# Kernel tuning notes

Hardware: AMD Instinct MI355X
Metric: run time of the kernel (lower is better)

Reference implementation:

```python
import jax, jax.numpy as jnp
import numpy as np

VOCAB = 16000
DIM = 1024
B, T = 4, 2048


def setup_inputs() -> dict:
    key = jax.random.key(0)
    k_ids, k_emb, k_w, k_lw, k_lb = jax.random.split(key, 5)
    input_ids = jax.random.randint(k_ids, (B, T), 0, VOCAB)
    embed = jax.random.normal(k_emb, (VOCAB, DIM), dtype=jnp.float32)
    # w_state = I + 0.05 * (default Linear init ~ U(-1/sqrt(dim), 1/sqrt(dim)))
    bound = 1.0 / np.sqrt(DIM)
    w_state = jnp.eye(DIM, dtype=jnp.float32) + 0.05 * jax.random.uniform(
        k_w, (DIM, DIM), minval=-bound, maxval=bound, dtype=jnp.float32)
    lm_w = jax.random.uniform(k_lw, (VOCAB, DIM), minval=-bound, maxval=bound, dtype=jnp.float32)
    lm_b = jax.random.uniform(k_lb, (VOCAB,), minval=-bound, maxval=bound, dtype=jnp.float32)
    return {"input_ids": input_ids, "embed": embed, "w_state": w_state,
            "lm_w": lm_w, "lm_b": lm_b}


def reference(input_ids, embed, w_state, lm_w, lm_b):
    # h: [B, T, D]
    h = embed[input_ids]
    state0 = jnp.zeros((h.shape[0], h.shape[2]), dtype=h.dtype)

    def step(state, h_t):
        # nn.Linear: state @ W^T ; then add input injection
        new_state = state @ w_state.T + h_t
        return new_state, new_state

    # scan over time: inputs [T, B, D]
    _, outs = jax.lax.scan(step, state0, jnp.swapaxes(h, 0, 1))
    hidden = jnp.swapaxes(outs, 0, 1)  # [B, T, D]
    logits = hidden @ lm_w.T + lm_b    # [B, T, V]
    return logits
```

## Files before the change

kernel.cpp:

```cpp
#include <hip/hip_runtime.h>
#include <hip/hip_bf16.h>
#include <stdint.h>

#define DD 1024
#define BB 4
#define TT 2048
#define VV 16000
#define LCH 8
#define NR 1024
#define PADR 512

typedef __bf16 bf16_t;
typedef float f32x4_t __attribute__((ext_vector_type(4)));
typedef bf16_t bf16x8_t __attribute__((ext_vector_type(8)));
typedef bf16_t bf16x4_t __attribute__((ext_vector_type(4)));

#define MODE_PLAIN 0
#define MODE_ROUND 1
#define MODE_LEVEL 2
#define MODE_CARRY 3

#define KIND_SQ 0
#define KIND_ROUND 1
#define KIND_LEVEL 2
#define KIND_CARRY 3

struct Job {
  const float* A; const float* B; float* C; const float* Cin;
  int kind; int dlt;
};
struct Jobs { Job j[8]; };

__global__ __launch_bounds__(256) void k_cvt(const float* __restrict__ src,
                                             bf16_t* __restrict__ dst, int n4) {
  int i = blockIdx.x * blockDim.x + threadIdx.x;
  int stride = gridDim.x * blockDim.x;
  for (; i < n4; i += stride) {
    float4 v = ((const float4*)src)[i];
    union { ushort4 u; bf16_t h[4]; } p;
    p.h[0] = (bf16_t)v.x; p.h[1] = (bf16_t)v.y;
    p.h[2] = (bf16_t)v.z; p.h[3] = (bf16_t)v.w;
    ((ushort4*)dst)[i] = p.u;
  }
}

__global__ __launch_bounds__(256) void k_gather(const float* __restrict__ embed,
                                                const int* __restrict__ ids,
                                                float* __restrict__ slab0) {
  int r = blockIdx.x;
  int b = r & 3, c = r >> 2;
  int id = ids[b * TT + c * LCH];
  const float4* s = (const float4*)(embed + (size_t)id * DD);
  float4* d = (float4*)(slab0 + (size_t)r * DD);
  for (int i = threadIdx.x; i < DD / 4; i += blockDim.x) d[i] = s[i];
}

template <int NS>
__device__ __forceinline__ void swrite(char* base, int byteoff, float4 v) {
  float r0 = v.x, r1 = v.y, r2 = v.z, r3 = v.w;
#pragma unroll
  for (int p = 0; p < NS; ++p) {
    bf16x4_t h;
    h[0] = (bf16_t)r0; h[1] = (bf16_t)r1; h[2] = (bf16_t)r2; h[3] = (bf16_t)r3;
    *(bf16x4_t*)(base + p * 5120 + byteoff) = h;
    if (p + 1 < NS) {
      r0 -= (float)h[0]; r1 -= (float)h[1]; r2 -= (float)h[2]; r3 -= (float)h[3];
    }
  }
}

template <int NS, bool NN, int MODE>
__device__ __forceinline__ void mbody(bf16_t* __restrict__ SB, const Job& jb,
                                      const float* __restrict__ embed,
                                      const int* __restrict__ ids,
                                      bf16_t* __restrict__ hidden) {
  const float* A = jb.A;
  const float* Bm = jb.B;
  const int tid = threadIdx.x, lane = tid & 63, wave = tid >> 6;
  const int i0 = blockIdx.y * 64, j0 = blockIdx.x * 64;
  const int wm = (wave >> 1) * 32, wn = (wave & 1) * 32;
  char* Ap = (char*)SB;
  char* Bp = Ap + NS * 5120;
  const int arow = tid >> 2;
  const int akb = (tid & 3) * 8;
  const int bj = tid & 63, bk4 = (tid >> 6) * 4;
  const int frow = lane & 15, fkb = (lane >> 4) * 16;
  f32x4_t acc[2][2] = {};

  const float* Aptr = A + (size_t)(i0 + arow) * DD + (tid & 3) * 4;
  const float* BptrNT = Bm + (size_t)(j0 + arow) * DD + (tid & 3) * 4;
  const float* BptrNN = Bm + (size_t)bk4 * DD + j0 + bj;

  float4 a0 = *(const float4*)(Aptr);
  float4 a1 = *(const float4*)(Aptr + 16);
  float4 b0, b1;
  float s0[4], s1[4];
  if (!NN) {
    b0 = *(const float4*)(BptrNT);
    b1 = *(const float4*)(BptrNT + 16);
  } else {
#pragma unroll
    for (int s = 0; s < 4; ++s) s0[s] = BptrNN[(size_t)s * DD];
#pragma unroll
    for (int s = 0; s < 4; ++s) s1[s] = BptrNN[(size_t)(16 + s) * DD];
  }

  for (int k0 = 0;;) {
    __syncthreads();
    swrite<NS>(Ap, arow * 80 + akb, a0);
    swrite<NS>(Ap, arow * 80 + akb + 32, a1);
    if (!NN) {
      swrite<NS>(Bp, arow * 80 + akb, b0);
      swrite<NS>(Bp, arow * 80 + akb + 32, b1);
    } else {
      float4 t0; t0.x = s0[0]; t0.y = s0[1]; t0.z = s0[2]; t0.w = s0[3];
      float4 t1; t1.x = s1[0]; t1.y = s1[1]; t1.z = s1[2]; t1.w = s1[3];
      swrite<NS>(Bp, bj * 80 + bk4 * 2, t0);
      swrite<NS>(Bp, bj * 80 + bk4 * 2 + 32, t1);
    }
    __syncthreads();
    int kn = k0 + 32;
    if (kn < DD) {
      a0 = *(const float4*)(Aptr + kn);
      a1 = *(const float4*)(Aptr + kn + 16);
      if (!NN) {
        b0 = *(const float4*)(BptrNT + kn);
        b1 = *(const float4*)(BptrNT + kn + 16);
      } else {
#pragma unroll
        for (int s = 0; s < 4; ++s) s0[s] = BptrNN[(size_t)(kn + s) * DD];
#pragma unroll
        for (int s = 0; s < 4; ++s) s1[s] = BptrNN[(size_t)(kn + 16 + s) * DD];
      }
    }
    bf16x8_t af[NS][2], bfx[NS][2];
#pragma unroll
    for (int p = 0; p < NS; ++p)
#pragma unroll
      for (int mf = 0; mf < 2; ++mf) {
        af[p][mf] = *(const bf16x8_t*)(Ap + p * 5120 + (wm + mf * 16 + frow) * 80 + fkb);
        bfx[p][mf] = *(const bf16x8_t*)(Bp + p * 5120 + (wn + mf * 16 + frow) * 80 + fkb);
      }
#pragma unroll
    for (int pa = 0; pa < NS; ++pa)
#pragma unroll
      for (int pb = 0; pb < NS; ++pb) {
        if (pa + pb < NS) {
#pragma unroll
          for (int mf = 0; mf < 2; ++mf)
#pragma unroll
            for (int nf = 0; nf < 2; ++nf)
              acc[mf][nf] = __builtin_amdgcn_mfma_f32_16x16x32_bf16(
                  af[pa][mf], bfx[pb][nf], acc[mf][nf], 0, 0, 0);
        }
      }
    k0 = kn;
    if (k0 >= DD) break;
  }

  const int ecol = lane & 15, er4 = (lane >> 4) * 4;
#pragma unroll
  for (int mf = 0; mf < 2; ++mf) {
#pragma unroll
    for (int nf = 0; nf < 2; ++nf) {
      const int rb = i0 + wm + mf * 16 + er4;
      const int cj = j0 + wn + nf * 16 + ecol;
#pragma unroll
      for (int rg = 0; rg < 4; ++rg) {
        const int ri = rb + rg;
        float v = acc[mf][nf][rg];
        if (MODE == MODE_PLAIN) {
          jb.C[(size_t)ri * DD + cj] = v;
        } else if (MODE == MODE_ROUND) {
          int b = ri & 3, c = ri >> 2, t = c * LCH + jb.dlt;
          v += embed[(size_t)ids[b * TT + t] * DD + cj];
          jb.C[(size_t)ri * DD + cj] = v;
        } else if (MODE == MODE_LEVEL) {
          v += jb.Cin[(size_t)ri * DD + cj];
          jb.C[(size_t)ri * DD + cj] = v;
        } else {
          int b = ri & 3, c = ri >> 2, t = c * LCH + jb.dlt;
          hidden[((size_t)b * TT + t) * DD + cj] =
              (bf16_t)(v + jb.Cin[(size_t)ri * DD + cj]);
        }
      }
    }
  }
}

__global__ __launch_bounds__(256, 2) void k_multi(Jobs jobs,
                                                  const float* __restrict__ embed,
                                                  const int* __restrict__ ids,
                                                  bf16_t* __restrict__ hidden) {
  __shared__ __align__(16) bf16_t SB[6 * 2560];
  const Job& jb = jobs.j[blockIdx.z];
  if (jb.kind == KIND_SQ)
    mbody<3, true, MODE_PLAIN>(SB, jb, embed, ids, hidden);
  else if (jb.kind == KIND_ROUND)
    mbody<2, false, MODE_ROUND>(SB, jb, embed, ids, hidden);
  else if (jb.kind == KIND_LEVEL)
    mbody<2, false, MODE_LEVEL>(SB, jb, embed, ids, hidden);
  else
    mbody<2, false, MODE_CARRY>(SB, jb, embed, ids, hidden);
}

__device__ __forceinline__ void gload16(const void* g, void* l) {
  __builtin_amdgcn_global_load_lds((const __attribute__((address_space(1))) void*)g,
                                   (__attribute__((address_space(3))) void*)l, 16, 0, 0);
}

__global__ __launch_bounds__(256) void k_lmhead(const bf16_t* __restrict__ Ah,
                                                const bf16_t* __restrict__ Bw,
                                                const float* __restrict__ bias,
                                                float* __restrict__ Cout) {
  __shared__ bf16_t Al[128 * 64];
  __shared__ bf16_t Bl[128 * 64];
  int orig = blockIdx.y * gridDim.x + blockIdx.x;
  int swz = (orig & 7) * 1000 + (orig >> 3);
  int bx = swz % 125, by = swz / 125;
  int m0 = by * 128, n0 = bx * 128;
  int tid = threadIdx.x;
  int wave = tid >> 6, lane = tid & 63;
  int wm = (wave >> 1) * 64, wn = (wave & 1) * 64;
  f32x4_t acc[4][4] = {};
  int frow = lane & 15;

  for (int k0 = 0; k0 < DD; k0 += 64) {
#pragma unroll
    for (int it = 0; it < 4; ++it) {
      int zb = it * 4096 + wave * 1024;
      int tpos = zb + lane * 16;
      int row = tpos >> 7;
      int scol = (tpos & 127) ^ ((row & 7) << 4);
      gload16((const char*)Ah + ((size_t)(m0 + row) * DD + k0) * 2 + scol,
              (char*)Al + zb);
      gload16((const char*)Bw + ((size_t)(n0 + row) * DD + k0) * 2 + scol,
              (char*)Bl + zb);
    }
    __syncthreads();
    bf16x8_t afr[2][4], bfr[2][4];
#pragma unroll
    for (int b = 0; b < 2; ++b) {
#pragma unroll
      for (int mf = 0; mf < 4; ++mf) {
        int r = wm + mf * 16 + frow;
        int off = (b * 64 + (lane >> 4) * 16) ^ ((r & 7) << 4);
        afr[b][mf] = *(const bf16x8_t*)((const char*)Al + r * 128 + off);
        int rn = wn + mf * 16 + frow;
        bfr[b][mf] = *(const bf16x8_t*)((const char*)Bl + rn * 128 + off);
      }
    }
#pragma unroll
    for (int b = 0; b < 2; ++b)
#pragma unroll
      for (int mf = 0; mf < 4; ++mf)
#pragma unroll
        for (int nf = 0; nf < 4; ++nf)
          acc[mf][nf] = __builtin_amdgcn_mfma_f32_16x16x32_bf16(
              afr[b][mf], bfr[b][nf], acc[mf][nf], 0, 0, 0);
    __syncthreads();
  }
  int ecol = lane & 15, erow4 = (lane >> 4) * 4;
#pragma unroll
  for (int mf = 0; mf < 4; ++mf) {
#pragma unroll
    for (int nf = 0; nf < 4; ++nf) {
      int gm = m0 + wm + mf * 16 + erow4;
      int gn = n0 + wn + nf * 16 + ecol;
      float bv = bias[gn];
#pragma unroll
      for (int reg = 0; reg < 4; ++reg)
        Cout[(size_t)(gm + reg) * VV + gn] = acc[mf][nf][reg] + bv;
    }
  }
}

extern "C" void kernel_launch(void* const* d_in, const int* in_sizes, int n_in,
                              void* d_out, int out_size, void* d_ws, size_t ws_size,
                              hipStream_t stream) {
  (void)in_sizes; (void)n_in; (void)out_size; (void)ws_size;
  const int* ids = (const int*)d_in[0];
  const float* embed = (const float*)d_in[1];
  const float* w_state = (const float*)d_in[2];
  const float* lm_w = (const float*)d_in[3];
  const float* lm_b = (const float*)d_in[4];
  float* out = (float*)d_out;

  const size_t M1 = (size_t)DD * DD;
  float* PW = (float*)d_ws;
  float* Q = PW + 8 * M1;
  float* LOC = Q + 7 * M1;
  float* E0 = LOC + 8 * M1;
  float* E1 = E0 + (size_t)(PADR + NR) * DD;
  bf16_t* HID = (bf16_t*)(E1 + (size_t)(PADR + NR) * DD);
  bf16_t* LWB = HID + (size_t)BB * TT * DD;
  float* E0d = E0 + (size_t)PADR * DD;
  float* E1d = E1 + (size_t)PADR * DD;

  k_cvt<<<2048, 256, 0, stream>>>(lm_w, LWB, VV * DD / 4);
  hipMemcpyAsync(PW, w_state, M1 * sizeof(float), hipMemcpyDeviceToDevice, stream);
  k_gather<<<NR, 256, 0, stream>>>(embed, ids, LOC);
  hipMemsetAsync(E0, 0, (size_t)PADR * DD * sizeof(float), stream);
  hipMemsetAsync(E1, 0, (size_t)PADR * DD * sizeof(float), stream);

  Jobs J{};
  J.j[0] = Job{w_state, w_state, PW + M1, nullptr, KIND_SQ, 0};
  J.j[1] = Job{LOC, w_state, LOC + M1, nullptr, KIND_ROUND, 1};
  k_multi<<<dim3(16, 16, 2), 256, 0, stream>>>(J, embed, ids, HID);
  J.j[0] = Job{PW + M1, w_state, PW + 2 * M1, nullptr, KIND_SQ, 0};
  J.j[1] = Job{PW + M1, PW + M1, PW + 3 * M1, nullptr, KIND_SQ, 0};
  J.j[2] = Job{LOC + M1, w_state, LOC + 2 * M1, nullptr, KIND_ROUND, 2};
  k_multi<<<dim3(16, 16, 3), 256, 0, stream>>>(J, embed, ids, HID);
  J.j[0] = Job{PW + 3 * M1, w_state, PW + 4 * M1, nullptr, KIND_SQ, 0};
  J.j[1] = Job{PW + 3 * M1, PW + M1, PW + 5 * M1, nullptr, KIND_SQ, 0};
  J.j[2] = Job{PW + 3 * M1, PW + 2 * M1, PW + 6 * M1, nullptr, KIND_SQ, 0};
  J.j[3] = Job{PW + 3 * M1, PW + 3 * M1, PW + 7 * M1, nullptr, KIND_SQ, 0};
  J.j[4] = Job{LOC + 2 * M1, w_state, LOC + 3 * M1, nullptr, KIND_ROUND, 3};
  k_multi<<<dim3(16, 16, 5), 256, 0, stream>>>(J, embed, ids, HID);
  for (int d = 4; d <= 7; ++d) {
    const float* src = (d == 4) ? (PW + 7 * M1) : (Q + (size_t)(d - 5) * M1);
    J.j[0] = Job{src, src, Q + (size_t)(d - 4) * M1, nullptr, KIND_SQ, 0};
    J.j[1] = Job{LOC + (size_t)(d - 1) * M1, w_state, LOC + (size_t)d * M1,
                 nullptr, KIND_ROUND, d};
    k_multi<<<dim3(16, 16, 2), 256, 0, stream>>>(J, embed, ids, HID);
  }
  hipMemcpyAsync(E0d, LOC + 7 * M1, M1 * sizeof(float),
                 hipMemcpyDeviceToDevice, stream);

  float* inp = E0d;
  float* outp = E1d;
  for (int k = 0; k < 8; ++k) {
    Jobs J2{};
    int nz = 0;
    if (k <= 2) {
      const float* src = Q + (size_t)(k + 3) * M1;
      J2.j[nz++] = Job{src, src, Q + (size_t)(k + 4) * M1, nullptr, KIND_SQ, 0};
    }
    const float* Bq = (k == 0) ? (PW + 7 * M1) : (Q + (size_t)(k - 1) * M1);
    J2.j[nz++] = Job{inp - (size_t)(4 << k) * DD, Bq, outp, inp, KIND_LEVEL, 0};
    k_multi<<<dim3(16, 16, nz), 256, 0, stream>>>(J2, embed, ids, HID);
    float* t = inp; inp = outp; outp = t;
  }

  Jobs Jc{};
  for (int d = 0; d < 8; ++d)
    Jc.j[d] = Job{inp - (size_t)4 * DD, PW + (size_t)d * M1, nullptr,
                  LOC + (size_t)d * M1, KIND_CARRY, d};
  k_multi<<<dim3(16, 16, 8), 256, 0, stream>>>(Jc, embed, ids, HID);

  dim3 gl(VV / 128, (BB * TT) / 128);
  k_lmhead<<<gl, 256, 0, stream>>>(HID, LWB, lm_b, out);
}
```

Baseline: 1.002 ms.

## Rewrite LM-head GEMM with 256x256 tiles and a 4-stage async LDS pipeline

```diff
diff --git a/kernel.cpp b/kernel.cpp
--- a/kernel.cpp
+++ b/kernel.cpp
@@ -9,6 +9,7 @@
 #define LCH 8
 #define NR 1024
 #define PADR 512
+#define NPAD 16128
 
 typedef __bf16 bf16_t;
 typedef float f32x4_t __attribute__((ext_vector_type(4)));
@@ -209,68 +210,100 @@
                                    (__attribute__((address_space(3))) void*)l, 16, 0, 0);
 }
 
-__global__ __launch_bounds__(256) void k_lmhead(const bf16_t* __restrict__ Ah,
-                                                const bf16_t* __restrict__ Bw,
-                                                const float* __restrict__ bias,
-                                                float* __restrict__ Cout) {
-  __shared__ bf16_t Al[128 * 64];
-  __shared__ bf16_t Bl[128 * 64];
+#define NTK 32
+
+__global__ __launch_bounds__(512, 2) void k_lmhead2(
+    const bf16_t* __restrict__ Ah, const bf16_t* __restrict__ Bw,
+    const float* __restrict__ bias, float* __restrict__ Cout) {
+  __shared__ __align__(16) char LB[4 * 32768];
+  const int tid = threadIdx.x, lane = tid & 63, wave = tid >> 6;
+  const int wr = wave >> 2, wc = wave & 3;
   int orig = blockIdx.y * gridDim.x + blockIdx.x;
-  int swz = (orig & 7) * 1000 + (orig >> 3);
-  int bx = swz % 125, by = swz / 125;
-  int m0 = by * 128, n0 = bx * 128;
-  int tid = threadIdx.x;
-  int wave = tid >> 6, lane = tid & 63;
-  int wm = (wave >> 1) * 64, wn = (wave & 1) * 64;
-  f32x4_t acc[4][4] = {};
-  int frow = lane & 15;
-
-  for (int k0 = 0; k0 < DD; k0 += 64) {
-#pragma unroll
-    for (int it = 0; it < 4; ++it) {
-      int zb = it * 4096 + wave * 1024;
-      int tpos = zb + lane * 16;
-      int row = tpos >> 7;
-      int scol = (tpos & 127) ^ ((row & 7) << 4);
-      gload16((const char*)Ah + ((size_t)(m0 + row) * DD + k0) * 2 + scol,
-              (char*)Al + zb);
-      gload16((const char*)Bw + ((size_t)(n0 + row) * DD + k0) * 2 + scol,
-              (char*)Bl + zb);
-    }
-    __syncthreads();
-    bf16x8_t afr[2][4], bfr[2][4];
-#pragma unroll
-    for (int b = 0; b < 2; ++b) {
-#pragma unroll
-      for (int mf = 0; mf < 4; ++mf) {
-        int r = wm + mf * 16 + frow;
-        int off = (b * 64 + (lane >> 4) * 16) ^ ((r & 7) << 4);
-        afr[b][mf] = *(const bf16x8_t*)((const char*)Al + r * 128 + off);
-        int rn = wn + mf * 16 + frow;
-        bfr[b][mf] = *(const bf16x8_t*)((const char*)Bl + rn * 128 + off);
-      }
-    }
-#pragma unroll
-    for (int b = 0; b < 2; ++b)
-#pragma unroll
-      for (int mf = 0; mf < 4; ++mf)
-#pragma unroll
-        for (int nf = 0; nf < 4; ++nf)
-          acc[mf][nf] = __builtin_amdgcn_mfma_f32_16x16x32_bf16(
-              afr[b][mf], bfr[b][nf], acc[mf][nf], 0, 0, 0);
-    __syncthreads();
-  }
-  int ecol = lane & 15, erow4 = (lane >> 4) * 4;
-#pragma unroll
-  for (int mf = 0; mf < 4; ++mf) {
+  int swz = (orig & 7) * 252 + (orig >> 3);
+  int by = swz / 63, bx = swz % 63;
+  const int m0 = by * 256, n0 = bx * 256;
+
+  const int srow = tid >> 2;
+  const int scb = (tid & 3) * 16;
+
+  auto stage = [&](int t) {
+    char* buf = LB + (size_t)(t & 3) * 32768;
+#pragma unroll
+    for (int p = 0; p < 2; ++p) {
+      int row = p * 128 + srow;
+      int sw = ((row >> 1) & 3) << 4;
+      gload16((const char*)Ah + ((size_t)(m0 + row) * DD + t * 32) * 2 + (scb ^ sw),
+              buf + p * 8192 + wave * 1024);
+      gload16((const char*)Bw + ((size_t)(n0 + row) * DD + t * 32) * 2 + (scb ^ sw),
+              buf + 16384 + p * 8192 + wave * 1024);
+    }
+  };
+
+  const int frow = lane & 15;
+  const int c4b = (lane >> 4) * 16;
+  f32x4_t acc[8][4] = {};
+
+  stage(0); stage(1); stage(2);
+  asm volatile("s_waitcnt vmcnt(8)\ns_barrier" ::: "memory");
+
+  for (int t = 0; t < NTK; ++t) {
+    char* Abuf = LB + (size_t)(t & 3) * 32768;
+    char* Bbuf = Abuf + 16384;
+    if (t + 3 < NTK) stage(t + 3);
+    bf16x8_t afr[4], bfr[4];
 #pragma unroll
     for (int nf = 0; nf < 4; ++nf) {
-      int gm = m0 + wm + mf * 16 + erow4;
-      int gn = n0 + wn + nf * 16 + ecol;
-      float bv = bias[gn];
-#pragma unroll
-      for (int reg = 0; reg < 4; ++reg)
-        Cout[(size_t)(gm + reg) * VV + gn] = acc[mf][nf][reg] + bv;
+      int r = wc * 64 + nf * 16 + frow;
+      bfr[nf] = *(const bf16x8_t*)(Bbuf + r * 64 + (c4b ^ (((r >> 1) & 3) << 4)));
+    }
+#pragma unroll
+    for (int mf = 0; mf < 4; ++mf) {
+      int r = wr * 128 + mf * 16 + frow;
+      afr[mf] = *(const bf16x8_t*)(Abuf + r * 64 + (c4b ^ (((r >> 1) & 3) << 4)));
+    }
+    __builtin_amdgcn_s_setprio(1);
+#pragma unroll
+    for (int mf = 0; mf < 4; ++mf)
+#pragma unroll
+      for (int nf = 0; nf < 4; ++nf)
+        acc[mf][nf] = __builtin_amdgcn_mfma_f32_16x16x32_bf16(
+            afr[mf], bfr[nf], acc[mf][nf], 0, 0, 0);
+    __builtin_amdgcn_s_setprio(0);
+#pragma unroll
+    for (int mf = 0; mf < 4; ++mf) {
+      int r = wr * 128 + 64 + mf * 16 + frow;
+      afr[mf] = *(const bf16x8_t*)(Abuf + r * 64 + (c4b ^ (((r >> 1) & 3) << 4)));
+    }
+    __builtin_amdgcn_s_setprio(1);
+#pragma unroll
+    for (int mf = 0; mf < 4; ++mf)
+#pragma unroll
+      for (int nf = 0; nf < 4; ++nf)
+        acc[4 + mf][nf] = __builtin_amdgcn_mfma_f32_16x16x32_bf16(
+            afr[mf], bfr[nf], acc[4 + mf][nf], 0, 0, 0);
+    __builtin_amdgcn_s_setprio(0);
+    if (t < NTK - 3) {
+      asm volatile("s_waitcnt vmcnt(8)\ns_barrier" ::: "memory");
+    } else if (t == NTK - 3) {
+      asm volatile("s_waitcnt vmcnt(4)\ns_barrier" ::: "memory");
+    } else if (t == NTK - 2) {
+      asm volatile("s_waitcnt vmcnt(0)\ns_barrier" ::: "memory");
+    }
+  }
+
+  const int ecol = lane & 15, er4 = (lane >> 4) * 4;
+#pragma unroll
+  for (int mf = 0; mf < 8; ++mf) {
+#pragma unroll
+    for (int nf = 0; nf < 4; ++nf) {
+      int gm = m0 + wr * 128 + mf * 16 + er4;
+      int gn = n0 + wc * 64 + nf * 16 + ecol;
+      if (gn < VV) {
+        float bv = bias[gn];
+#pragma unroll
+        for (int rg = 0; rg < 4; ++rg)
+          Cout[(size_t)(gm + rg) * VV + gn] = acc[mf][nf][rg] + bv;
+      }
     }
   }
 }
@@ -298,6 +331,8 @@
   float* E1d = E1 + (size_t)PADR * DD;
 
   k_cvt<<<2048, 256, 0, stream>>>(lm_w, LWB, VV * DD / 4);
+  hipMemsetAsync(LWB + (size_t)VV * DD, 0,
+                 (size_t)(NPAD - VV) * DD * sizeof(bf16_t), stream);
   hipMemcpyAsync(PW, w_state, M1 * sizeof(float), hipMemcpyDeviceToDevice, stream);
   k_gather<<<NR, 256, 0, stream>>>(embed, ids, LOC);
   hipMemsetAsync(E0, 0, (size_t)PADR * DD * sizeof(float), stream);
@@ -348,6 +383,6 @@
                   LOC + (size_t)d * M1, KIND_CARRY, d};
   k_multi<<<dim3(16, 16, 8), 256, 0, stream>>>(Jc, embed, ids, HID);
 
-  dim3 gl(VV / 128, (BB * TT) / 128);
-  k_lmhead<<<gl, 256, 0, stream>>>(HID, LWB, lm_b, out);
-}
+  dim3 gl(NPAD / 256, (BB * TT) / 256);
+  k_lmhead2<<<gl, 512, 0, stream>>>(HID, LWB, lm_b, out);
+}
```

Measured after the change: 900.1 us. 1.11x faster.
